# Optimization experiments

Hardware: AMD Instinct MI355X
Metric: run time of the kernel (lower is better)

The kernel has to match this reference:

```python
import jax, jax.numpy as jnp
import numpy as np

N, M, D = 8192, 8192, 256
GAMMA = 1.0 / D  # standard RBF bandwidth gamma = 1/D


def setup_inputs() -> dict:
    key = jax.random.key(0)
    kx, ks = jax.random.split(key)
    x = jax.random.normal(kx, (N, D), dtype=jnp.float32)
    support = jax.random.normal(ks, (M, D), dtype=jnp.float32)
    return {"x": x, "support": support}


def reference(x, support):
    # Vectorized RBF Gram matrix: K[i, j] = exp(-gamma * ||x_i - s_j||^2)
    # ||x_i - s_j||^2 = ||x_i||^2 + ||s_j||^2 - 2 x_i . s_j  (cdist-style, one GEMM)
    x_sq = jnp.sum(x * x, axis=-1, keepdims=True)            # [N, 1]
    s_sq = jnp.sum(support * support, axis=-1)[None, :]      # [1, M]
    cross = jnp.einsum('nd,md->nm', x, support)              # [N, M]
    sq_dists = jnp.maximum(x_sq + s_sq - 2.0 * cross, 0.0)   # clamp fp error
    return jnp.exp(-GAMMA * sq_dists)
```

## Files before the change

### kernel.cpp

```cpp
#include <hip/hip_runtime.h>

#define N 8192
#define M 8192
#define D 256

typedef unsigned short ushort_t;
typedef __attribute__((ext_vector_type(8))) short short8;
typedef __attribute__((ext_vector_type(4))) float floatx4;

__device__ __forceinline__ unsigned short f2bf(float f) {
  unsigned int u = __float_as_uint(f);
  u += 0x7fffu + ((u >> 16) & 1u);
  return (unsigned short)(u >> 16);
}

__global__ __launch_bounds__(256) void prep_kernel(const float* __restrict__ x,
                                                   const float* __restrict__ s,
                                                   ushort_t* __restrict__ xb,
                                                   ushort_t* __restrict__ sb,
                                                   float* __restrict__ xn,
                                                   float* __restrict__ sn) {
  int gw = blockIdx.x * 4 + (threadIdx.x >> 6);
  int lane = threadIdx.x & 63;
  const float* src;
  ushort_t* dst;
  float* nrm;
  int row;
  if (gw < N) { src = x; dst = xb; nrm = xn; row = gw; }
  else        { src = s; dst = sb; nrm = sn; row = gw - N; }
  float4 v = ((const float4*)(src + (size_t)row * D))[lane];
  float ss = v.x * v.x + v.y * v.y + v.z * v.z + v.w * v.w;
  ushort4 o;
  o.x = f2bf(v.x); o.y = f2bf(v.y); o.z = f2bf(v.z); o.w = f2bf(v.w);
  const int g = row >> 6;
  const int sub = (row >> 4) & 3;
  const int m = row & 15;
  const int c = lane >> 3;
  const int q = (lane >> 1) & 3;
  size_t off = (size_t)g * 32768 +
               (size_t)((c * 4 + sub) * 1024 + q * 256 + m * 16 + (lane & 1) * 8);
  *(ushort4*)((char*)dst + off) = o;
#pragma unroll
  for (int offs = 32; offs > 0; offs >>= 1) ss += __shfl_down(ss, offs);
  if (lane == 0) nrm[row] = ss;
}

__global__ __launch_bounds__(256, 2) void rbf_gemm(const ushort_t* __restrict__ X,
                                                   const ushort_t* __restrict__ S,
                                                   const float* __restrict__ xn,
                                                   const float* __restrict__ sn,
                                                   float* __restrict__ out) {
  __shared__ __attribute__((aligned(16))) ushort_t As[4 * 128 * 32];
  __shared__ __attribute__((aligned(16))) ushort_t Bs[4 * 128 * 32];
  __shared__ float xnS[128];
  __shared__ float snS[128];

  const int tid = threadIdx.x;
  const int lane = tid & 63;
  const int wave = tid >> 6;
  const int bx = blockIdx.x;
  const int by = blockIdx.y;

  if (tid < 128) xnS[tid] = xn[by * 128 + tid];
  else           snS[tid - 128] = sn[bx * 128 + (tid - 128)];

  const int wr = (wave >> 1) * 64;
  const int wc = (wave & 1) * 64;
  const int q4 = lane >> 4;
  const int m16 = lane & 15;

  const char* gAb = (const char*)X + (size_t)by * 65536 + lane * 16;
  const char* gBb = (const char*)S + (size_t)bx * 65536 + lane * 16;
  char* lAb = (char*)As + wave * 8192;
  char* lBb = (char*)Bs + wave * 8192;

  floatx4 acc[4][4];
#pragma unroll
  for (int i = 0; i < 4; ++i)
#pragma unroll
    for (int j = 0; j < 4; ++j) acc[i][j] = (floatx4){0.f, 0.f, 0.f, 0.f};

#pragma unroll
  for (int r = 0; r < 2; ++r) {
    const int kc4 = (r * 4 + wave) * 4;
    __syncthreads();
#pragma unroll
    for (int sub = 0; sub < 8; ++sub) {
      const size_t gsel = (size_t)(sub >> 2) * 32768;
      const int s4 = sub & 3;
      __builtin_amdgcn_global_load_lds(
          (const __attribute__((address_space(1))) void*)(gAb + gsel + ((kc4 + s4) << 10)),
          (__attribute__((address_space(3))) void*)(lAb + (sub << 10)), 16, 0, 0);
      __builtin_amdgcn_global_load_lds(
          (const __attribute__((address_space(1))) void*)(gBb + gsel + ((kc4 + s4) << 10)),
          (__attribute__((address_space(3))) void*)(lBb + (sub << 10)), 16, 0, 0);
    }
    __syncthreads();

#pragma unroll
    for (int c = 0; c < 4; ++c) {
      const char* cA = (const char*)As + c * 8192 + lane * 16;
      const char* cB = (const char*)Bs + c * 8192 + lane * 16;
      short8 a_frag[4], b_frag[4];
#pragma unroll
      for (int i = 0; i < 4; ++i)
        a_frag[i] = *(const short8*)(cA + ((wave >> 1) * 4 + i) * 1024);
#pragma unroll
      for (int j = 0; j < 4; ++j)
        b_frag[j] = *(const short8*)(cB + ((wave & 1) * 4 + j) * 1024);
#pragma unroll
      for (int i = 0; i < 4; ++i)
#pragma unroll
        for (int j = 0; j < 4; ++j)
          acc[i][j] = __builtin_amdgcn_mfma_f32_16x16x32_bf16(a_frag[i], b_frag[j],
                                                              acc[i][j], 0, 0, 0);
    }
  }

  const float cexp = -1.0f / (float)D;
#pragma unroll
  for (int i = 0; i < 4; ++i) {
#pragma unroll
    for (int j = 0; j < 4; ++j) {
#pragma unroll
      for (int r = 0; r < 4; ++r) {
        const int rl = wr + i * 16 + q4 * 4 + r;
        const int cl = wc + j * 16 + m16;
        float sq = xnS[rl] + snS[cl] - 2.0f * acc[i][j][r];
        sq = fmaxf(sq, 0.0f);
        out[(size_t)(by * 128 + rl) * M + (bx * 128 + cl)] = __expf(cexp * sq);
      }
    }
  }
}

extern "C" void kernel_launch(void* const* d_in, const int* in_sizes, int n_in,
                              void* d_out, int out_size, void* d_ws, size_t ws_size,
                              hipStream_t stream) {
  const float* x = (const float*)d_in[0];
  const float* s = (const float*)d_in[1];
  float* out = (float*)d_out;
  char* ws = (char*)d_ws;
  ushort_t* xb = (ushort_t*)ws;
  ushort_t* sb = (ushort_t*)(ws + (size_t)N * D * 2);
  float* xn = (float*)(ws + (size_t)(N + M) * D * 2);
  float* sn = xn + N;

  prep_kernel<<<(N + M) / 4, 256, 0, stream>>>(x, s, xb, sb, xn, sn);
  dim3 grid(M / 128, N / 128);
  rbf_gemm<<<grid, 256, 0, stream>>>(xb, sb, xn, sn, out);
}
```

Measured before the change: 295.2 us.

## Double-buffer K-loop LDS staging and fold RBF scaling into exp2 epilogue

Restructures the GEMM main loop from two fully synchronized load-then-compute rounds into four rounds with double-buffered LDS, so the next round's global-to-LDS loads overlap the current round's MFMA work. The norms are prescaled by -log2(e)/D in the prep kernel, which turns the epilogue into a single fma, a min and a native exp2. The norms are also read straight from global memory into registers instead of going through shared memory. The cost is more synchronization points and smaller stages, and the 32 KB per buffer pair is unchanged in total LDS use.

Result: no change. 299.9 us (+1.6%).

```diff
diff --git a/kernel.cpp b/kernel.cpp
--- a/kernel.cpp
+++ b/kernel.cpp
@@ -3,6 +3,7 @@
 #define N 8192
 #define M 8192
 #define D 256
+#define LOG2E 1.44269504088896340736f
 
 typedef unsigned short ushort_t;
 typedef __attribute__((ext_vector_type(8))) short short8;
@@ -42,7 +43,55 @@
   *(ushort4*)((char*)dst + off) = o;
 #pragma unroll
   for (int offs = 32; offs > 0; offs >>= 1) ss += __shfl_down(ss, offs);
-  if (lane == 0) nrm[row] = ss;
+  if (lane == 0) nrm[row] = ss * (-LOG2E / (float)D);
+}
+
+__device__ __forceinline__ void stage_round(const char* gX, const char* gS,
+                                            ushort_t* lA, ushort_t* lB,
+                                            int t, int wave, int lane) {
+#pragma unroll
+  for (int i = 0; i < 4; ++i) {
+    const int tt = wave * 4 + i;
+    const int g = tt >> 3, c32 = (tt >> 2) & 1, sub = tt & 3;
+    const size_t goff = (size_t)g * 32768 +
+                        (size_t)(((2 * t + c32) * 4 + sub) * 1024) + lane * 16;
+    __builtin_amdgcn_global_load_lds(
+        (const __attribute__((address_space(1))) void*)(gX + goff),
+        (__attribute__((address_space(3))) void*)((char*)lA + tt * 1024), 16, 0, 0);
+    __builtin_amdgcn_global_load_lds(
+        (const __attribute__((address_space(1))) void*)(gS + goff),
+        (__attribute__((address_space(3))) void*)((char*)lB + tt * 1024), 16, 0, 0);
+  }
+}
+
+__device__ __forceinline__ void compute_round(const ushort_t* __restrict__ As_,
+                                              const ushort_t* __restrict__ Bs_,
+                                              floatx4 (&acc)[4][4], int wave,
+                                              int lane) {
+  const int pa = (wave >> 1) * 4;
+  const int pb = (wave & 1) * 4;
+#pragma unroll
+  for (int c32 = 0; c32 < 2; ++c32) {
+    short8 a_frag[4], b_frag[4];
+#pragma unroll
+    for (int i = 0; i < 4; ++i) {
+      const int p = pa + i;
+      a_frag[i] = *(const short8*)((const char*)As_ +
+                  (((p >> 2) * 8 + c32 * 4 + (p & 3)) * 1024) + lane * 16);
+    }
+#pragma unroll
+    for (int j = 0; j < 4; ++j) {
+      const int p = pb + j;
+      b_frag[j] = *(const short8*)((const char*)Bs_ +
+                  (((p >> 2) * 8 + c32 * 4 + (p & 3)) * 1024) + lane * 16);
+    }
+#pragma unroll
+    for (int i = 0; i < 4; ++i)
+#pragma unroll
+      for (int j = 0; j < 4; ++j)
+        acc[i][j] = __builtin_amdgcn_mfma_f32_16x16x32_bf16(a_frag[i], b_frag[j],
+                                                            acc[i][j], 0, 0, 0);
+  }
 }
 
 __global__ __launch_bounds__(256, 2) void rbf_gemm(const ushort_t* __restrict__ X,
@@ -50,10 +99,8 @@
                                                    const float* __restrict__ xn,
                                                    const float* __restrict__ sn,
                                                    float* __restrict__ out) {
-  __shared__ __attribute__((aligned(16))) ushort_t As[4 * 128 * 32];
-  __shared__ __attribute__((aligned(16))) ushort_t Bs[4 * 128 * 32];
-  __shared__ float xnS[128];
-  __shared__ float snS[128];
+  __shared__ __attribute__((aligned(16))) ushort_t As[2][8192];
+  __shared__ __attribute__((aligned(16))) ushort_t Bs[2][8192];
 
   const int tid = threadIdx.x;
   const int lane = tid & 63;
@@ -61,18 +108,8 @@
   const int bx = blockIdx.x;
   const int by = blockIdx.y;
 
-  if (tid < 128) xnS[tid] = xn[by * 128 + tid];
-  else           snS[tid - 128] = sn[bx * 128 + (tid - 128)];
-
-  const int wr = (wave >> 1) * 64;
-  const int wc = (wave & 1) * 64;
-  const int q4 = lane >> 4;
-  const int m16 = lane & 15;
-
-  const char* gAb = (const char*)X + (size_t)by * 65536 + lane * 16;
-  const char* gBb = (const char*)S + (size_t)bx * 65536 + lane * 16;
-  char* lAb = (char*)As + wave * 8192;
-  char* lBb = (char*)Bs + wave * 8192;
+  const char* gX = (const char*)X + (size_t)by * 65536;
+  const char* gS = (const char*)S + (size_t)bx * 65536;
 
   floatx4 acc[4][4];
 #pragma unroll
@@ -80,44 +117,32 @@
 #pragma unroll
     for (int j = 0; j < 4; ++j) acc[i][j] = (floatx4){0.f, 0.f, 0.f, 0.f};
 
-#pragma unroll
-  for (int r = 0; r < 2; ++r) {
-    const int kc4 = (r * 4 + wave) * 4;
-    __syncthreads();
-#pragma unroll
-    for (int sub = 0; sub < 8; ++sub) {
-      const size_t gsel = (size_t)(sub >> 2) * 32768;
-      const int s4 = sub & 3;
-      __builtin_amdgcn_global_load_lds(
-          (const __attribute__((address_space(1))) void*)(gAb + gsel + ((kc4 + s4) << 10)),
-          (__attribute__((address_space(3))) void*)(lAb + (sub << 10)), 16, 0, 0);
-      __builtin_amdgcn_global_load_lds(
-          (const __attribute__((address_space(1))) void*)(gBb + gsel + ((kc4 + s4) << 10)),
-          (__attribute__((address_space(3))) void*)(lBb + (sub << 10)), 16, 0, 0);
-    }
-    __syncthreads();
+  stage_round(gX, gS, As[0], Bs[0], 0, wave, lane);
+  __syncthreads();
 
 #pragma unroll
-    for (int c = 0; c < 4; ++c) {
-      const char* cA = (const char*)As + c * 8192 + lane * 16;
-      const char* cB = (const char*)Bs + c * 8192 + lane * 16;
-      short8 a_frag[4], b_frag[4];
-#pragma unroll
-      for (int i = 0; i < 4; ++i)
-        a_frag[i] = *(const short8*)(cA + ((wave >> 1) * 4 + i) * 1024);
-#pragma unroll
-      for (int j = 0; j < 4; ++j)
-        b_frag[j] = *(const short8*)(cB + ((wave & 1) * 4 + j) * 1024);
-#pragma unroll
-      for (int i = 0; i < 4; ++i)
-#pragma unroll
-        for (int j = 0; j < 4; ++j)
-          acc[i][j] = __builtin_amdgcn_mfma_f32_16x16x32_bf16(a_frag[i], b_frag[j],
-                                                              acc[i][j], 0, 0, 0);
-    }
+  for (int t = 0; t < 4; ++t) {
+    if (t < 3)
+      stage_round(gX, gS, As[(t + 1) & 1], Bs[(t + 1) & 1], t + 1, wave, lane);
+    compute_round(As[t & 1], Bs[t & 1], acc, wave, lane);
+    if (t < 3)
+      __syncthreads();
   }
 
-  const float cexp = -1.0f / (float)D;
+  const int wr = (wave >> 1) * 64;
+  const int wc = (wave & 1) * 64;
+  const int q4 = lane >> 4;
+  const int m16 = lane & 15;
+
+  floatx4 rowA[4];
+  const float* xrow = xn + by * 128 + wr + q4 * 4;
+#pragma unroll
+  for (int i = 0; i < 4; ++i) rowA[i] = *(const floatx4*)(xrow + i * 16);
+  float colB[4];
+#pragma unroll
+  for (int j = 0; j < 4; ++j) colB[j] = sn[bx * 128 + wc + j * 16 + m16];
+
+  const float k2 = 2.0f * LOG2E / (float)D;
 #pragma unroll
   for (int i = 0; i < 4; ++i) {
 #pragma unroll
@@ -126,9 +151,9 @@
       for (int r = 0; r < 4; ++r) {
         const int rl = wr + i * 16 + q4 * 4 + r;
         const int cl = wc + j * 16 + m16;
-        float sq = xnS[rl] + snS[cl] - 2.0f * acc[i][j][r];
-        sq = fmaxf(sq, 0.0f);
-        out[(size_t)(by * 128 + rl) * M + (bx * 128 + cl)] = __expf(cexp * sq);
+        float arg = fminf(fmaf(k2, acc[i][j][r], rowA[i][r] + colB[j]), 0.0f);
+        out[(size_t)(by * 128 + rl) * M + (bx * 128 + cl)] =
+            __builtin_amdgcn_exp2f(arg);
       }
     }
   }
```
